# Kernel tuning notes

Hardware: AMD Instinct MI355X
Metric: run time of the kernel (lower is better)

Reference implementation:

```python
import jax, jax.numpy as jnp
import numpy as np

EPS = 1e-12


def _l2norm(x):
    # F.normalize(x, dim=1): x / max(||x||, eps)
    n = jnp.sqrt(jnp.sum(x * x, axis=1, keepdims=True))
    return x / jnp.maximum(n, EPS)


def _remove_diag(x):
    # x: [n, n] -> [n, n-1], dropping the diagonal (matches x[~eye].view(n, -1))
    n = x.shape[0]
    row = jnp.arange(n)[:, None]
    base = jnp.arange(n - 1)[None, :]
    cols = jnp.where(base < row, base, base + 1)  # column indices != row index
    return jnp.take_along_axis(x, cols, axis=1)


def _lid_mle(data, reference, k):
    # pairwise euclidean distances [n_data, n_ref]
    d2 = (jnp.sum(data * data, axis=1)[:, None]
          + jnp.sum(reference * reference, axis=1)[None, :]
          - 2.0 * data @ reference.T)
    dist = jnp.sqrt(jnp.maximum(d2, 0.0))
    # k+1 smallest distances (index 0 is the self-distance since data subset of reference)
    neg_top, _ = jax.lax.top_k(-dist, k + 1)
    d = -neg_top[:, 1:]  # [n, k], ascending, self excluded
    # MLE LID estimator: -k / sum_i log(d_i / d_k)
    return -k / jnp.sum(jnp.log(d / d[:, -1:] + EPS), axis=1)


def _byol_loss(p, z):
    z = jax.lax.stop_gradient(z)
    return 2.0 - 2.0 * jnp.sum(_l2norm(p) * _l2norm(z), axis=1)


def _track_logits(o0, o1):
    b = o0.shape[0]
    l00 = _remove_diag(jnp.einsum('nc,mc->nm', o0, o0))
    l01 = jnp.einsum('nc,mc->nm', o0, o1)
    l10 = jnp.einsum('nc,mc->nm', o1, o0)
    l11 = _remove_diag(jnp.einsum('nc,mc->nm', o1, o1))
    logits = jnp.concatenate([
        jnp.concatenate([l01, l00], axis=1),
        jnp.concatenate([l10, l11], axis=1)], axis=0)  # [2b, 2b-1]
    labels = jnp.tile(jnp.arange(b, dtype=jnp.int32), 2)
    return logits, labels


def setup_inputs() -> dict:
    key = jax.random.key(0)
    ks = jax.random.split(key, 9)
    B, Dfe, Dp, C = 4096, 2048, 256, 1000
    return {
        'fe_0': jax.random.normal(ks[0], (B, Dfe), jnp.float32),
        'fe_1': jax.random.normal(ks[1], (B, Dfe), jnp.float32),
        'p_0': jax.random.normal(ks[2], (B, Dp), jnp.float32),
        'p_1': jax.random.normal(ks[3], (B, Dp), jnp.float32),
        'z_0': jax.random.normal(ks[4], (B, Dp), jnp.float32),
        'z_1': jax.random.normal(ks[5], (B, Dp), jnp.float32),
        'cls_0': jax.random.normal(ks[6], (B, C), jnp.float32),
        'cls_1': jax.random.normal(ks[7], (B, C), jnp.float32),
        'online_labels': jax.random.randint(ks[8], (B,), 0, C, jnp.int32),
    }


def reference(fe_0, fe_1, p_0, p_1, z_0, z_1, cls_0, cls_1, online_labels):
    # BYOL symmetric loss
    main_loss = jnp.mean(_byol_loss(p_0, z_1) + _byol_loss(p_1, z_0))
    # online linear-probe cross-entropy on concatenated views
    cls = jnp.concatenate([cls_0, cls_1], axis=0)
    labels2 = jnp.concatenate([online_labels, online_labels], axis=0)
    logp = jax.nn.log_softmax(cls, axis=1)
    online_loss = -jnp.mean(jnp.take_along_axis(logp, labels2[:, None], axis=1)[:, 0])
    # LID tracking on backbone features (no-grad in original)
    fe = jnp.concatenate([fe_0, fe_1], axis=0)
    lids32 = _lid_mle(fe, fe, 32)
    lids512 = _lid_mle(fe, fe, 512)
    # contrastive-style logit tracking on normalized predictor outputs
    logits, labels = _track_logits(_l2norm(p_0), _l2norm(p_1))
    return main_loss, online_loss, logits, labels, lids32, lids512
```

## Files before the change

### kernel.cpp

```cpp
#include <hip/hip_runtime.h>
#include <math.h>

typedef __bf16 bf16;
typedef __bf16 bf16x8 __attribute__((ext_vector_type(8)));
typedef __bf16 bf16x4 __attribute__((ext_vector_type(4)));
typedef float f32x4 __attribute__((ext_vector_type(4)));

#define NROW 8192
#define BHALF 4096
#define DFE 2048
#define DP 256
#define NCLS 1000

#define LOGITS_N 8191
#define OUT_LOGITS 2
#define OUT_LABELS (2 + 8192 * 8191)
#define OUT_LIDS32 (OUT_LABELS + 8192)
#define OUT_LIDS512 (OUT_LIDS32 + 8192)

#define G0TILES 1056
#define G1TILES 2048

__device__ inline void gload16(const bf16* g, bf16* l) {
    __builtin_amdgcn_global_load_lds((const __attribute__((address_space(1))) void*)g,
                                     (__attribute__((address_space(3))) void*)l, 16, 0, 0);
}

__global__ __launch_bounds__(256) void init_kernel(float* out) {
    int i = blockIdx.x * 256 + threadIdx.x;
    if (i < 2) out[i] = 0.f;
    if (i < NROW) out[(size_t)OUT_LABELS + i] = (float)(i & (BHALF - 1));
}

__global__ __launch_bounds__(256) void split_fe_kernel(const float* __restrict__ fe0,
                                                       const float* __restrict__ fe1,
                                                       bf16* __restrict__ feh,
                                                       bf16* __restrict__ fel,
                                                       float* __restrict__ norms) {
    int row = blockIdx.x, tid = threadIdx.x;
    const float* src = (row < BHALF) ? fe0 + (size_t)row * DFE
                                     : fe1 + (size_t)(row - BHALF) * DFE;
    float ss = 0.f;
#pragma unroll
    for (int pass = 0; pass < 2; ++pass) {
        int c = (pass * 256 + tid) * 4;
        float4 v = *(const float4*)(src + c);
        ss += v.x * v.x + v.y * v.y + v.z * v.z + v.w * v.w;
        bf16 h0 = (bf16)v.x, h1 = (bf16)v.y, h2 = (bf16)v.z, h3 = (bf16)v.w;
        bf16 l0 = (bf16)(v.x - (float)h0), l1 = (bf16)(v.y - (float)h1);
        bf16 l2 = (bf16)(v.z - (float)h2), l3 = (bf16)(v.w - (float)h3);
        bf16x4 hv = {h0, h1, h2, h3};
        bf16x4 lv = {l0, l1, l2, l3};
        *(bf16x4*)(feh + (size_t)row * DFE + c) = hv;
        *(bf16x4*)(fel + (size_t)row * DFE + c) = lv;
    }
#pragma unroll
    for (int off = 32; off; off >>= 1) ss += __shfl_down(ss, off);
    __shared__ float red[4];
    if ((tid & 63) == 0) red[tid >> 6] = ss;
    __syncthreads();
    if (tid == 0) norms[row] = red[0] + red[1] + red[2] + red[3];
}

__global__ __launch_bounds__(256) void norm_split_p_kernel(const float* __restrict__ p0,
                                                           const float* __restrict__ p1,
                                                           bf16* __restrict__ oh) {
    int row = blockIdx.x, tid = threadIdx.x;
    const float* src = (row < BHALF) ? p0 + (size_t)row * DP
                                     : p1 + (size_t)(row - BHALF) * DP;
    float x = src[tid];
    float ss = x * x;
#pragma unroll
    for (int off = 32; off; off >>= 1) ss += __shfl_down(ss, off);
    __shared__ float red[4];
    if ((tid & 63) == 0) red[tid >> 6] = ss;
    __syncthreads();
    float tot = red[0] + red[1] + red[2] + red[3];
    float rn = 1.f / fmaxf(sqrtf(tot), 1e-12f);
    oh[(size_t)row * DP + tid] = (bf16)(x * rn);
}

__device__ inline float dot4(float4 a, float4 b) {
    return a.x * b.x + a.y * b.y + a.z * b.z + a.w * b.w;
}

__global__ __launch_bounds__(256) void byol_kernel(const float* __restrict__ p0,
                                                   const float* __restrict__ p1,
                                                   const float* __restrict__ z0,
                                                   const float* __restrict__ z1,
                                                   float* out) {
    int tid = threadIdx.x, wave = tid >> 6, lane = tid & 63;
    int row = blockIdx.x * 4 + wave;
    size_t base = (size_t)row * DP + lane * 4;
    float4 a0 = *(const float4*)(p0 + base);
    float4 b0 = *(const float4*)(z1 + base);
    float4 a1 = *(const float4*)(p1 + base);
    float4 b1 = *(const float4*)(z0 + base);
    float pp0 = dot4(a0, a0), zz0 = dot4(b0, b0), pz0 = dot4(a0, b0);
    float pp1 = dot4(a1, a1), zz1 = dot4(b1, b1), pz1 = dot4(a1, b1);
#pragma unroll
    for (int off = 32; off; off >>= 1) {
        pp0 += __shfl_down(pp0, off); zz0 += __shfl_down(zz0, off); pz0 += __shfl_down(pz0, off);
        pp1 += __shfl_down(pp1, off); zz1 += __shfl_down(zz1, off); pz1 += __shfl_down(pz1, off);
    }
    __shared__ float red[4];
    if (lane == 0) {
        float c0 = pz0 / (fmaxf(sqrtf(pp0), 1e-12f) * fmaxf(sqrtf(zz0), 1e-12f));
        float c1 = pz1 / (fmaxf(sqrtf(pp1), 1e-12f) * fmaxf(sqrtf(zz1), 1e-12f));
        red[wave] = (2.f - 2.f * c0) + (2.f - 2.f * c1);
    }
    __syncthreads();
    if (tid == 0) atomicAdd(out, (red[0] + red[1] + red[2] + red[3]) * (1.f / 4096.f));
}

__global__ __launch_bounds__(256) void online_kernel(const float* __restrict__ cls0,
                                                     const float* __restrict__ cls1,
                                                     const int* __restrict__ labels,
                                                     float* out) {
    int tid = threadIdx.x, wave = tid >> 6, lane = tid & 63;
    int row = blockIdx.x * 4 + wave;
    const float* src = (row < BHALF) ? cls0 + (size_t)row * NCLS
                                     : cls1 + (size_t)(row - BHALF) * NCLS;
    int lbl = labels[row & (BHALF - 1)];
    float xs[16];
    float mx = -INFINITY;
#pragma unroll
    for (int j = 0; j < 16; ++j) {
        int c = lane + j * 64;
        xs[j] = (c < NCLS) ? src[c] : -INFINITY;
        mx = fmaxf(mx, xs[j]);
    }
#pragma unroll
    for (int off = 32; off; off >>= 1) mx = fmaxf(mx, __shfl_xor(mx, off));
    float se = 0.f;
#pragma unroll
    for (int j = 0; j < 16; ++j) se += expf(xs[j] - mx);
#pragma unroll
    for (int off = 32; off; off >>= 1) se += __shfl_xor(se, off);
    __shared__ float red[4];
    if (lane == 0) red[wave] = src[lbl] - mx - logf(se);
    __syncthreads();
    if (tid == 0) atomicAdd(out + 1, -(red[0] + red[1] + red[2] + red[3]) * (1.f / 8192.f));
}

__device__ inline void stage_half(const bf16* __restrict__ mat, int Kd, int rowbase,
                                  int k0, bf16* lds, int wave, int rsub, int lg) {
#pragma unroll
    for (int q = 0; q < 2; ++q)
        gload16(mat + (size_t)(rowbase + q * 64 + wave * 8 + rsub) * Kd + k0 + lg * 8,
                lds + (q * 64 + wave * 8) * 64);
}

__global__ __launch_bounds__(512, 2) void gemm_kernel(const bf16* __restrict__ Hp,
                                                      const bf16* __restrict__ Lp,
                                                      const bf16* __restrict__ OHp,
                                                      const float* __restrict__ norms,
                                                      float* __restrict__ d2,
                                                      float* __restrict__ outlog) {
    __shared__ bf16 sm[2][24576];
    int tid = threadIdx.x, lane = tid & 63, wave = tid >> 6;
    int wr = wave >> 1, wc = wave & 1;
    int lrow = lane & 15, lquad = lane >> 4, r7 = lrow & 7, pg = lquad ^ r7;
    int rsub = lane >> 3, grp = lane & 7, lg = grp ^ rsub;

    int bid = blockIdx.x;
    int mode, tm, tn, ksh;
    const bf16 *Hmat, *Lmat;
    int Kd;
    if (bid < G0TILES) {
        mode = 0;
        int sw = (bid & 7) * (G0TILES / 8) + (bid >> 3);
        int i = 0;
        while ((i + 1) * (65 - (i + 1)) <= sw) ++i;
        tm = i;
        tn = 2 * i + (sw - i * (65 - i));
        Hmat = Hp; Lmat = Lp; Kd = DFE; ksh = 5;
    } else {
        mode = 1;
        int id = bid - G0TILES;
        int sw = (id & 7) * (G1TILES / 8) + (id >> 3);
        tm = sw & 31; tn = sw >> 5;
        Hmat = OHp; Lmat = OHp; Kd = DP; ksh = 2;
    }
    int NT = (mode == 0 ? 3 : 1) << ksh;
    int kmask = (1 << ksh) - 1;
    int arow0 = tm * 256, brow0 = tn * 128;

    f32x4 acc[4][4];
    f32x4 zz = {0.f, 0.f, 0.f, 0.f};
#pragma unroll
    for (int i = 0; i < 4; ++i)
#pragma unroll
        for (int j = 0; j < 4; ++j) acc[i][j] = zz;

    stage_half(Hmat, Kd, arow0, 0, sm[0], wave, rsub, lg);
    stage_half(Hmat, Kd, brow0, 0, sm[0] + 16384, wave, rsub, lg);
    stage_half(Hmat, Kd, arow0 + 128, 0, sm[0] + 8192, wave, rsub, lg);
    stage_half(Hmat, Kd, arow0, 64, sm[1], wave, rsub, lg);
    stage_half(Hmat, Kd, brow0, 64, sm[1] + 16384, wave, rsub, lg);
    asm volatile("s_waitcnt vmcnt(6)" ::: "memory");
    __builtin_amdgcn_s_barrier();

    bf16x8 bfr[4][2];
    for (int gt = 0; gt < NT; ++gt) {
        int cur = gt & 1;
        const char* Sb = (const char*)sm[cur];
        const bf16 *A1m = Hmat, *A2m = Hmat, *B2m = Hmat;
        int k01 = 0, k02 = 0;
        if (gt + 1 < NT) {
            int nt = gt + 1, ch = nt >> ksh;
            k01 = (nt & kmask) * 64;
            A1m = (ch == 1) ? Lmat : Hmat;
        }
        if (gt + 2 < NT) {
            int nt = gt + 2, ch = nt >> ksh;
            k02 = (nt & kmask) * 64;
            A2m = (ch == 1) ? Lmat : Hmat;
            B2m = (ch == 2) ? Lmat : Hmat;
        }

        bf16x8 af[2][2];
#pragma unroll
        for (int ii = 0; ii < 2; ++ii) {
            int off = ((ii * 4 + wr) * 16 + lrow) * 128 + pg * 16;
            af[ii][0] = *(const bf16x8*)(Sb + off);
            af[ii][1] = *(const bf16x8*)(Sb + (off ^ 64));
        }
#pragma unroll
        for (int j = 0; j < 4; ++j) {
            int off = 32768 + ((j * 2 + wc) * 16 + lrow) * 128 + pg * 16;
            bfr[j][0] = *(const bf16x8*)(Sb + off);
            bfr[j][1] = *(const bf16x8*)(Sb + (off ^ 64));
        }
        if (gt + 1 < NT)
            stage_half(A1m, Kd, arow0 + 128, k01, sm[cur ^ 1] + 8192, wave, rsub, lg);
        __builtin_amdgcn_s_barrier();
        asm volatile("s_waitcnt lgkmcnt(0)" ::: "memory");
        __builtin_amdgcn_sched_barrier(0);
        __builtin_amdgcn_s_setprio(1);
#pragma unroll
        for (int ii = 0; ii < 2; ++ii)
#pragma unroll
            for (int j = 0; j < 4; ++j) {
                acc[ii][j] = __builtin_amdgcn_mfma_f32_16x16x32_bf16(af[ii][0], bfr[j][0], acc[ii][j], 0, 0, 0);
                acc[ii][j] = __builtin_amdgcn_mfma_f32_16x16x32_bf16(af[ii][1], bfr[j][1], acc[ii][j], 0, 0, 0);
            }
        __builtin_amdgcn_s_setprio(0);
        if (gt + 1 < NT) asm volatile("s_waitcnt vmcnt(6)" ::: "memory");
        else             asm volatile("s_waitcnt vmcnt(0)" ::: "memory");
        __builtin_amdgcn_s_barrier();

#pragma unroll
        for (int ii = 0; ii < 2; ++ii) {
            int off = (((ii + 2) * 4 + wr) * 16 + lrow) * 128 + pg * 16;
            af[ii][0] = *(const bf16x8*)(Sb + off);
            af[ii][1] = *(const bf16x8*)(Sb + (off ^ 64));
        }
        if (gt + 2 < NT) {
            stage_half(A2m, Kd, arow0, k02, sm[cur], wave, rsub, lg);
            stage_half(B2m, Kd, brow0, k02, sm[cur] + 16384, wave, rsub, lg);
        }
        __builtin_amdgcn_s_barrier();
        asm volatile("s_waitcnt lgkmcnt(0)" ::: "memory");
        __builtin_amdgcn_sched_barrier(0);
        __builtin_amdgcn_s_setprio(1);
#pragma unroll
        for (int ii = 0; ii < 2; ++ii)
#pragma unroll
            for (int j = 0; j < 4; ++j) {
                acc[ii + 2][j] = __builtin_amdgcn_mfma_f32_16x16x32_bf16(af[ii][0], bfr[j][0], acc[ii + 2][j], 0, 0, 0);
                acc[ii + 2][j] = __builtin_amdgcn_mfma_f32_16x16x32_bf16(af[ii][1], bfr[j][1], acc[ii + 2][j], 0, 0, 0);
            }
        __builtin_amdgcn_s_setprio(0);
        if (gt + 2 < NT)      asm volatile("s_waitcnt vmcnt(6)" ::: "memory");
        else if (gt + 1 < NT) asm volatile("s_waitcnt vmcnt(2)" ::: "memory");
        __builtin_amdgcn_s_barrier();
    }

    if (mode == 0) {
#pragma unroll
        for (int i = 0; i < 4; ++i) {
#pragma unroll
            for (int e = 0; e < 4; ++e) {
                int grow = arow0 + (i * 4 + wr) * 16 + lquad * 4 + e;
                float na = norms[grow];
#pragma unroll
                for (int j = 0; j < 4; ++j) {
                    int gcol = tn * 128 + (j * 2 + wc) * 16 + lrow;
                    float v = na + norms[gcol] - 2.f * acc[i][j][e];
                    d2[(size_t)grow * NROW + gcol] = fmaxf(v, 0.f);
                }
            }
        }
    } else {
#pragma unroll
        for (int i = 0; i < 4; ++i) {
#pragma unroll
            for (int j = 0; j < 4; ++j) {
#pragma unroll
                for (int e = 0; e < 4; ++e) {
                    int r = arow0 + (i * 4 + wr) * 16 + lquad * 4 + e;
                    int c = tn * 128 + (j * 2 + wc) * 16 + lrow;
                    int oc = 0;
                    bool skip = false;
                    if (r < BHALF) {
                        if (c >= BHALF) oc = c - BHALF;
                        else if (c == r) skip = true;
                        else oc = BHALF + (c < r ? c : c - 1);
                    } else {
                        int rp = r - BHALF;
                        if (c < BHALF) oc = c;
                        else {
                            int cp = c - BHALF;
                            if (cp == rp) skip = true;
                            else oc = BHALF + (cp < rp ? cp : cp - 1);
                        }
                    }
                    if (!skip) outlog[(size_t)r * LOGITS_N + oc] = acc[i][j][e];
                }
            }
        }
    }
}

__global__ __launch_bounds__(256) void mirror_kernel(float* __restrict__ d2) {
    int bj = blockIdx.x, bi = blockIdx.y;
    if (bi < bj) return;
    __shared__ float t[32][33];
    int tx = threadIdx.x & 31, ty = threadIdx.x >> 5;
#pragma unroll
    for (int r = 0; r < 32; r += 8)
        t[r + ty][tx] = d2[(size_t)(bj * 32 + r + ty) * NROW + bi * 32 + tx];
    __syncthreads();
#pragma unroll
    for (int r = 0; r < 32; r += 8) {
        int gi = bi * 32 + r + ty, gj = bj * 32 + tx;
        if (gi > gj) d2[(size_t)gi * NROW + gj] = t[tx][r + ty];
    }
}

__global__ __launch_bounds__(256) void select_kernel(const float* __restrict__ d2,
                                                     float* __restrict__ out) {
    int wave = threadIdx.x >> 6, lane = threadIdx.x & 63;
    int row = blockIdx.x * 4 + wave;
    const float4* drow4 = (const float4*)(d2 + (size_t)row * NROW);
    unsigned v[128];
    unsigned andv = 0xFFFFFFFFu, orv = 0u;
#pragma unroll
    for (int j = 0; j < 32; ++j) {
        int idx4 = j * 64 + lane;
        float4 f = drow4[idx4];
        int c0 = idx4 * 4;
        unsigned u0 = __float_as_uint(f.x), u1 = __float_as_uint(f.y);
        unsigned u2 = __float_as_uint(f.z), u3 = __float_as_uint(f.w);
        bool s0 = (c0 == row), s1 = (c0 + 1 == row), s2 = (c0 + 2 == row), s3 = (c0 + 3 == row);
        v[j * 4 + 0] = s0 ? 0xFFFFFFFFu : u0;
        v[j * 4 + 1] = s1 ? 0xFFFFFFFFu : u1;
        v[j * 4 + 2] = s2 ? 0xFFFFFFFFu : u2;
        v[j * 4 + 3] = s3 ? 0xFFFFFFFFu : u3;
        andv &= (s0 ? 0xFFFFFFFFu : u0); orv |= (s0 ? 0u : u0);
        andv &= (s1 ? 0xFFFFFFFFu : u1); orv |= (s1 ? 0u : u1);
        andv &= (s2 ? 0xFFFFFFFFu : u2); orv |= (s2 ? 0u : u2);
        andv &= (s3 ? 0xFFFFFFFFu : u3); orv |= (s3 ? 0u : u3);
    }
#pragma unroll
    for (int off = 32; off; off >>= 1) {
        andv &= __shfl_xor(andv, off);
        orv |= __shfl_xor(orv, off);
    }
    unsigned diff = andv ^ orv;
    int msb = 31 - __clz((int)(diff | 1u));
    unsigned common = (msb == 31) ? 0u : (andv & (0xFFFFFFFFu << (msb + 1)));
    unsigned p1 = common, p2 = common;
    for (int bit = msb; bit >= 0; --bit) {
        unsigned c1 = p1 | (1u << bit), c2 = p2 | (1u << bit);
        unsigned n1 = 0, n2 = 0;
#pragma unroll
        for (int j = 0; j < 128; ++j) { n1 += (v[j] < c1); n2 += (v[j] < c2); }
#pragma unroll
        for (int off = 32; off; off >>= 1) {
            n1 += __shfl_xor(n1, off);
            n2 += __shfl_xor(n2, off);
        }
        if (n1 < 32u) p1 = c1;
        if (n2 < 512u) p2 = c2;
    }
    float dk1 = sqrtf(__uint_as_float(p1));
    float dk2 = sqrtf(__uint_as_float(p2));
    float s1 = 0.f, s2 = 0.f;
#pragma unroll
    for (int j = 0; j < 128; ++j) {
        unsigned b = v[j];
        if (b < p2) {
            float d = sqrtf(__uint_as_float(b));
            s2 += logf(d / dk2 + 1e-12f);
            if (b < p1) s1 += logf(d / dk1 + 1e-12f);
        }
    }
#pragma unroll
    for (int off = 32; off; off >>= 1) {
        s1 += __shfl_xor(s1, off);
        s2 += __shfl_xor(s2, off);
    }
    if (lane == 0) {
        out[(size_t)OUT_LIDS32 + row] = -32.f / s1;
        out[(size_t)OUT_LIDS512 + row] = -512.f / s2;
    }
}

extern "C" void kernel_launch(void* const* d_in, const int* in_sizes, int n_in,
                              void* d_out, int out_size, void* d_ws, size_t ws_size,
                              hipStream_t stream) {
    const float* fe0 = (const float*)d_in[0];
    const float* fe1 = (const float*)d_in[1];
    const float* p0 = (const float*)d_in[2];
    const float* p1 = (const float*)d_in[3];
    const float* z0 = (const float*)d_in[4];
    const float* z1 = (const float*)d_in[5];
    const float* cls0 = (const float*)d_in[6];
    const float* cls1 = (const float*)d_in[7];
    const int* labels = (const int*)d_in[8];
    float* out = (float*)d_out;

    char* ws = (char*)d_ws;
    float* D2 = (float*)ws;
    bf16* FEH = (bf16*)(ws + 268435456UL);
    bf16* FEL = (bf16*)(ws + 268435456UL + 33554432UL);
    bf16* OH = (bf16*)(ws + 268435456UL + 2 * 33554432UL);
    float* NORMS = (float*)(ws + 268435456UL + 2 * 33554432UL + 4194304UL);

    init_kernel<<<32, 256, 0, stream>>>(out);
    split_fe_kernel<<<8192, 256, 0, stream>>>(fe0, fe1, FEH, FEL, NORMS);
    norm_split_p_kernel<<<8192, 256, 0, stream>>>(p0, p1, OH);
    byol_kernel<<<1024, 256, 0, stream>>>(p0, p1, z0, z1, out);
    online_kernel<<<2048, 256, 0, stream>>>(cls0, cls1, labels, out);
    gemm_kernel<<<G0TILES + G1TILES, 512, 0, stream>>>(FEH, FEL, OH, NORMS, D2, out + OUT_LOGITS);
    mirror_kernel<<<dim3(256, 256), 256, 0, stream>>>(D2);
    select_kernel<<<2048, 256, 0, stream>>>(D2, out);
}
```

Before: 1.287 ms.

## Restructure GEMM main loop into register double-buffered, two-stage-unrolled pipeline

The GEMM main loop is unrolled by two k-steps. The full A and B fragments for the next LDS buffer are now read into a second register set while MFMAs run on the current set, replacing the old half-tile split where A rows were loaded in two phases. Global staging addresses are precomputed once as per-row base pointers plus a Lmat-Hmat delta, and LDS fragment offsets are hoisted. The aim is to overlap LDS reads with MFMA work and cut address arithmetic. In exchange it doubles fragment register usage, which may pressure occupancy under launch_bounds(512,2), and the vmcnt and barrier logic is reworked.

Measured after the change: 1.252 ms. -2.7%, faster.

```diff
diff --git a/kernel.cpp b/kernel.cpp
--- a/kernel.cpp
+++ b/kernel.cpp
@@ -141,14 +141,6 @@
     if (lane == 0) red[wave] = src[lbl] - mx - logf(se);
     __syncthreads();
     if (tid == 0) atomicAdd(out + 1, -(red[0] + red[1] + red[2] + red[3]) * (1.f / 8192.f));
-}
-
-__device__ inline void stage_half(const bf16* __restrict__ mat, int Kd, int rowbase,
-                                  int k0, bf16* lds, int wave, int rsub, int lg) {
-#pragma unroll
-    for (int q = 0; q < 2; ++q)
-        gload16(mat + (size_t)(rowbase + q * 64 + wave * 8 + rsub) * Kd + k0 + lg * 8,
-                lds + (q * 64 + wave * 8) * 64);
 }
 
 __global__ __launch_bounds__(512, 2) void gemm_kernel(const bf16* __restrict__ Hp,
@@ -185,6 +177,25 @@
     int NT = (mode == 0 ? 3 : 1) << ksh;
     int kmask = (1 << ksh) - 1;
     int arow0 = tm * 256, brow0 = tn * 128;
+    size_t delta = (size_t)(Lmat - Hmat);
+
+    const bf16* baseA[4];
+    const bf16* baseB[2];
+#pragma unroll
+    for (int q = 0; q < 4; ++q)
+        baseA[q] = Hmat + (size_t)(arow0 + q * 64 + wave * 8 + rsub) * Kd + lg * 8;
+#pragma unroll
+    for (int q = 0; q < 2; ++q)
+        baseB[q] = Hmat + (size_t)(brow0 + q * 64 + wave * 8 + rsub) * Kd + lg * 8;
+
+    int aoff[4], boff[4];
+#pragma unroll
+    for (int t = 0; t < 4; ++t) {
+        aoff[t] = (((t * 4 + wr) * 16 + lrow) * 64) * 2 + pg * 16;
+        boff[t] = 32768 + (((t * 2 + wc) * 16 + lrow) * 64) * 2 + pg * 16;
+    }
+    const char* S0 = (const char*)sm[0];
+    const char* S1 = (const char*)sm[1];
 
     f32x4 acc[4][4];
     f32x4 zz = {0.f, 0.f, 0.f, 0.f};
@@ -193,88 +204,82 @@
 #pragma unroll
         for (int j = 0; j < 4; ++j) acc[i][j] = zz;
 
-    stage_half(Hmat, Kd, arow0, 0, sm[0], wave, rsub, lg);
-    stage_half(Hmat, Kd, brow0, 0, sm[0] + 16384, wave, rsub, lg);
-    stage_half(Hmat, Kd, arow0 + 128, 0, sm[0] + 8192, wave, rsub, lg);
-    stage_half(Hmat, Kd, arow0, 64, sm[1], wave, rsub, lg);
-    stage_half(Hmat, Kd, brow0, 64, sm[1] + 16384, wave, rsub, lg);
+#define STAGE(nt, B)                                                        \
+    do {                                                                    \
+        int ch_ = (nt) >> ksh;                                              \
+        int k_ = ((nt) & kmask) << 6;                                       \
+        size_t dA_ = (ch_ == 1) ? delta : 0;                                \
+        size_t dB_ = (ch_ == 2) ? delta : 0;                                \
+        _Pragma("unroll") for (int q = 0; q < 4; ++q)                       \
+            gload16(baseA[q] + dA_ + k_, (B) + q * 4096 + wave * 512);      \
+        _Pragma("unroll") for (int q = 0; q < 2; ++q)                       \
+            gload16(baseB[q] + dB_ + k_, (B) + 16384 + q * 4096 + wave * 512); \
+    } while (0)
+
+#define READF(AF, BF, SB)                                                   \
+    do {                                                                    \
+        _Pragma("unroll") for (int t = 0; t < 4; ++t) {                     \
+            AF[t][0] = *(const bf16x8*)((SB) + aoff[t]);                    \
+            AF[t][1] = *(const bf16x8*)((SB) + (aoff[t] ^ 64));             \
+        }                                                                   \
+        _Pragma("unroll") for (int t = 0; t < 4; ++t) {                     \
+            BF[t][0] = *(const bf16x8*)((SB) + boff[t]);                    \
+            BF[t][1] = *(const bf16x8*)((SB) + (boff[t] ^ 64));             \
+        }                                                                   \
+    } while (0)
+
+#define MFMAC(AF, BF)                                                       \
+    do {                                                                    \
+        __builtin_amdgcn_s_setprio(1);                                      \
+        _Pragma("unroll") for (int i = 0; i < 4; ++i)                       \
+            _Pragma("unroll") for (int j = 0; j < 4; ++j) {                 \
+                acc[i][j] = __builtin_amdgcn_mfma_f32_16x16x32_bf16(AF[i][0], BF[j][0], acc[i][j], 0, 0, 0); \
+                acc[i][j] = __builtin_amdgcn_mfma_f32_16x16x32_bf16(AF[i][1], BF[j][1], acc[i][j], 0, 0, 0); \
+            }                                                               \
+        __builtin_amdgcn_s_setprio(0);                                      \
+    } while (0)
+
+    bf16x8 af0[4][2], bf0[4][2], af1[4][2], bf1[4][2];
+
+    STAGE(0, sm[0]);
+    STAGE(1, sm[1]);
     asm volatile("s_waitcnt vmcnt(6)" ::: "memory");
     __builtin_amdgcn_s_barrier();
-
-    bf16x8 bfr[4][2];
-    for (int gt = 0; gt < NT; ++gt) {
-        int cur = gt & 1;
-        const char* Sb = (const char*)sm[cur];
-        const bf16 *A1m = Hmat, *A2m = Hmat, *B2m = Hmat;
-        int k01 = 0, k02 = 0;
-        if (gt + 1 < NT) {
-            int nt = gt + 1, ch = nt >> ksh;
-            k01 = (nt & kmask) * 64;
-            A1m = (ch == 1) ? Lmat : Hmat;
-        }
-        if (gt + 2 < NT) {
-            int nt = gt + 2, ch = nt >> ksh;
-            k02 = (nt & kmask) * 64;
-            A2m = (ch == 1) ? Lmat : Hmat;
-            B2m = (ch == 2) ? Lmat : Hmat;
-        }
-
-        bf16x8 af[2][2];
-#pragma unroll
-        for (int ii = 0; ii < 2; ++ii) {
-            int off = ((ii * 4 + wr) * 16 + lrow) * 128 + pg * 16;
-            af[ii][0] = *(const bf16x8*)(Sb + off);
-            af[ii][1] = *(const bf16x8*)(Sb + (off ^ 64));
-        }
-#pragma unroll
-        for (int j = 0; j < 4; ++j) {
-            int off = 32768 + ((j * 2 + wc) * 16 + lrow) * 128 + pg * 16;
-            bfr[j][0] = *(const bf16x8*)(Sb + off);
-            bfr[j][1] = *(const bf16x8*)(Sb + (off ^ 64));
-        }
-        if (gt + 1 < NT)
-            stage_half(A1m, Kd, arow0 + 128, k01, sm[cur ^ 1] + 8192, wave, rsub, lg);
-        __builtin_amdgcn_s_barrier();
+    __builtin_amdgcn_sched_barrier(0);
+    READF(af0, bf0, S0);
+
+    for (int t = 0; t < NT; t += 2) {
         asm volatile("s_waitcnt lgkmcnt(0)" ::: "memory");
         __builtin_amdgcn_sched_barrier(0);
-        __builtin_amdgcn_s_setprio(1);
-#pragma unroll
-        for (int ii = 0; ii < 2; ++ii)
-#pragma unroll
-            for (int j = 0; j < 4; ++j) {
-                acc[ii][j] = __builtin_amdgcn_mfma_f32_16x16x32_bf16(af[ii][0], bfr[j][0], acc[ii][j], 0, 0, 0);
-                acc[ii][j] = __builtin_amdgcn_mfma_f32_16x16x32_bf16(af[ii][1], bfr[j][1], acc[ii][j], 0, 0, 0);
-            }
-        __builtin_amdgcn_s_setprio(0);
-        if (gt + 1 < NT) asm volatile("s_waitcnt vmcnt(6)" ::: "memory");
-        else             asm volatile("s_waitcnt vmcnt(0)" ::: "memory");
         __builtin_amdgcn_s_barrier();
-
-#pragma unroll
-        for (int ii = 0; ii < 2; ++ii) {
-            int off = (((ii + 2) * 4 + wr) * 16 + lrow) * 128 + pg * 16;
-            af[ii][0] = *(const bf16x8*)(Sb + off);
-            af[ii][1] = *(const bf16x8*)(Sb + (off ^ 64));
-        }
-        if (gt + 2 < NT) {
-            stage_half(A2m, Kd, arow0, k02, sm[cur], wave, rsub, lg);
-            stage_half(B2m, Kd, brow0, k02, sm[cur] + 16384, wave, rsub, lg);
+        if (t + 2 < NT) {
+            STAGE(t + 2, sm[0]);
+            asm volatile("s_waitcnt vmcnt(6)" ::: "memory");
+        } else {
+            asm volatile("s_waitcnt vmcnt(0)" ::: "memory");
         }
         __builtin_amdgcn_s_barrier();
+        __builtin_amdgcn_sched_barrier(0);
+        READF(af1, bf1, S1);
+        __builtin_amdgcn_sched_barrier(0);
+        MFMAC(af0, bf0);
+
         asm volatile("s_waitcnt lgkmcnt(0)" ::: "memory");
         __builtin_amdgcn_sched_barrier(0);
-        __builtin_amdgcn_s_setprio(1);
-#pragma unroll
-        for (int ii = 0; ii < 2; ++ii)
-#pragma unroll
-            for (int j = 0; j < 4; ++j) {
-                acc[ii + 2][j] = __builtin_amdgcn_mfma_f32_16x16x32_bf16(af[ii][0], bfr[j][0], acc[ii + 2][j], 0, 0, 0);
-                acc[ii + 2][j] = __builtin_amdgcn_mfma_f32_16x16x32_bf16(af[ii][1], bfr[j][1], acc[ii + 2][j], 0, 0, 0);
-            }
-        __builtin_amdgcn_s_setprio(0);
-        if (gt + 2 < NT)      asm volatile("s_waitcnt vmcnt(6)" ::: "memory");
-        else if (gt + 1 < NT) asm volatile("s_waitcnt vmcnt(2)" ::: "memory");
         __builtin_amdgcn_s_barrier();
+        if (t + 3 < NT) {
+            STAGE(t + 3, sm[1]);
+            asm volatile("s_waitcnt vmcnt(6)" ::: "memory");
+        } else if (t + 2 < NT) {
+            asm volatile("s_waitcnt vmcnt(0)" ::: "memory");
+        }
+        __builtin_amdgcn_s_barrier();
+        if (t + 2 < NT) {
+            __builtin_amdgcn_sched_barrier(0);
+            READF(af0, bf0, S0);
+            __builtin_amdgcn_sched_barrier(0);
+        }
+        MFMAC(af1, bf1);
     }
 
     if (mode == 0) {
@@ -321,6 +326,9 @@
             }
         }
     }
+#undef STAGE
+#undef READF
+#undef MFMAC
 }
 
 __global__ __launch_bounds__(256) void mirror_kernel(float* __restrict__ d2) {
```
